# Optimization experiments

Hardware: AMD Instinct MI355X
Metric: run time of the kernel (lower is better)

## Reference

```python
import jax, jax.numpy as jnp
import numpy as np

B, S, H, A = 32, 4096, 512, 256

def setup_inputs() -> dict:
    key = jax.random.key(0)
    ks = jax.random.split(key, 8)
    sH = 1.0 / np.sqrt(H)
    sA = 1.0 / np.sqrt(A)
    return {
        "encoder_outputs": jax.random.normal(ks[0], (B, S, H), dtype=jnp.float32),
        "decoder_hidden": jax.random.normal(ks[1], (B, H), dtype=jnp.float32),
        "W_enc": jax.random.uniform(ks[2], (H, A), jnp.float32, -sH, sH),
        "b_enc": jax.random.uniform(ks[3], (A,), jnp.float32, -sH, sH),
        "W_dec": jax.random.uniform(ks[4], (H, A), jnp.float32, -sH, sH),
        "b_dec": jax.random.uniform(ks[5], (A,), jnp.float32, -sH, sH),
        "W_e": jax.random.uniform(ks[6], (A,), jnp.float32, -sA, sA),
        "b_e": jax.random.uniform(ks[7], (), jnp.float32, -sA, sA),
    }

def reference(encoder_outputs, decoder_hidden, W_enc, b_enc, W_dec, b_dec, W_e, b_e):
    # [B,S,A] encoder projection
    enc_p = jnp.einsum('bsh,ha->bsa', encoder_outputs, W_enc) + b_enc
    # [B,1,A] decoder projection broadcast over S
    dec_p = (decoder_hidden @ W_dec + b_dec)[:, None, :]
    scores = jnp.einsum('bsa,a->bs', jnp.tanh(enc_p + dec_p), W_e) + b_e  # [B,S]
    attn = jax.nn.softmax(scores, axis=1)                                 # [B,S]
    context = jnp.einsum('bs,bsh->bh', attn, encoder_outputs)             # [B,H]
    return context, attn
```

## Files before the change

kernel.cpp:

```cpp
#include <hip/hip_runtime.h>
#include <hip/hip_bf16.h>
#include <stdint.h>


typedef __attribute__((ext_vector_type(4))) float f32x4;
typedef __attribute__((ext_vector_type(8))) short short8;

#define B_  32
#define S_  4096
#define H_  512
#define A_  256
#define CHUNKS_ 64

#define WS_WT     0
#define WS_BIAS   262144
#define WS_SCORES 294912
#define WS_M      819200
#define WS_L      827392
#define WS_PART   835584

#define STRIDE_ 520

static __device__ __forceinline__ short f2bf(float f) {
  union { float f; uint32_t u; } v; v.f = f;
  uint32_t r = (v.u + 0x7FFFu + ((v.u >> 16) & 1u)) >> 16;
  return (short)(uint16_t)r;
}
static __device__ __forceinline__ float bf2f(uint32_t lo16) {
  union { uint32_t u; float f; } v; v.u = lo16 << 16; return v.f;
}

static __device__ __forceinline__ void lds_barrier() {
  asm volatile("s_waitcnt lgkmcnt(0)" ::: "memory");
  __builtin_amdgcn_s_barrier();
  asm volatile("" ::: "memory");
}

__global__ __launch_bounds__(256) void prep_kernel(
    const float* __restrict__ dh, const float* __restrict__ W_enc,
    const float* __restrict__ b_enc, const float* __restrict__ W_dec,
    const float* __restrict__ b_dec, unsigned short* __restrict__ WT,
    float* __restrict__ bias) {
  __shared__ float dh_s[512];
  __shared__ unsigned short tile[64 * 66];
  const int tid = threadIdx.x;
  if (blockIdx.x < 32) {
    const int b = blockIdx.x;
    dh_s[tid]       = dh[(size_t)b * H_ + tid];
    dh_s[tid + 256] = dh[(size_t)b * H_ + tid + 256];
    __syncthreads();
    float s[4] = {0.f, 0.f, 0.f, 0.f};
    for (int k = 0; k < H_; k += 32) {
      #pragma unroll
      for (int j = 0; j < 32; ++j)
        s[j & 3] = fmaf(dh_s[k + j], W_dec[(size_t)(k + j) * A_ + tid], s[j & 3]);
    }
    bias[b * A_ + tid] = s[0] + s[1] + s[2] + s[3] + b_enc[tid] + b_dec[tid];
  } else {
    const int t = blockIdx.x - 32;
    const int kt = t >> 2, nt2 = t & 3;
    #pragma unroll
    for (int i = 0; i < 16; ++i) {
      int idx = tid + i * 256;
      int kk = idx >> 6, nn = idx & 63;
      tile[kk * 66 + nn] =
          (unsigned short)f2bf(W_enc[(size_t)(kt * 64 + kk) * A_ + nt2 * 64 + nn]);
    }
    __syncthreads();
    #pragma unroll
    for (int i = 0; i < 16; ++i) {
      int idx = tid + i * 256;
      int nn = idx >> 6, kk = idx & 63;
      WT[(size_t)(nt2 * 64 + nn) * H_ + kt * 64 + kk] = tile[kk * 66 + nn];
    }
  }
}

__global__ __launch_bounds__(256, 2) void fused_kernel(
    const float* __restrict__ enc, const unsigned short* __restrict__ WT,
    const float* __restrict__ bias, const float* __restrict__ We,
    float* __restrict__ scores, float* __restrict__ wsm,
    float* __restrict__ wsl, float* __restrict__ part) {
  __shared__ __align__(16) unsigned short stash[64 * STRIDE_];
  __shared__ float s_ps[4][64];
  __shared__ float s_e[64];

  const int tid = threadIdx.x, w = tid >> 6, lane = tid & 63;
  const int lm = lane & 15, lq = lane >> 4;
  const int b = blockIdx.x >> 6;
  const int chunk = blockIdx.x & 63;
  const int srow0 = blockIdx.x * 64;

  f32x4 acc[4][4];
  #pragma unroll
  for (int mt = 0; mt < 4; ++mt)
    #pragma unroll
    for (int nt = 0; nt < 4; ++nt)
      acc[mt][nt] = (f32x4){0.f, 0.f, 0.f, 0.f};

  const int arow = tid >> 2, akoff = (tid & 3) * 8;
  const float* aptr = enc + (size_t)(srow0 + arow) * H_ + akoff;
  unsigned short* swp = &stash[arow * STRIDE_ + akoff];

  const unsigned short* bptr = WT + (size_t)((w * 4) * 16 + lm) * H_ + lq * 8;

  short8 Bring[3][4];
  float4 Aring[3][2];

  float4 a0a = *(const float4*)aptr;
  float4 a0b = *(const float4*)(aptr + 4);
  Aring[1][0] = *(const float4*)(aptr + 1 * 32);
  Aring[1][1] = *(const float4*)(aptr + 1 * 32 + 4);
  Aring[2][0] = *(const float4*)(aptr + 2 * 32);
  Aring[2][1] = *(const float4*)(aptr + 2 * 32 + 4);
  #pragma unroll
  for (int j = 0; j < 4; ++j) {
    Bring[0][j] = *(const short8*)(bptr + (size_t)j * 16 * H_);
    Bring[1][j] = *(const short8*)(bptr + (size_t)j * 16 * H_ + 32);
  }
  {
    short8 sv;
    sv[0] = f2bf(a0a.x); sv[1] = f2bf(a0a.y); sv[2] = f2bf(a0a.z); sv[3] = f2bf(a0a.w);
    sv[4] = f2bf(a0b.x); sv[5] = f2bf(a0b.y); sv[6] = f2bf(a0b.z); sv[7] = f2bf(a0b.w);
    *(short8*)swp = sv;
  }
  lds_barrier();

  #pragma unroll
  for (int k = 0; k < 16; ++k) {
    if (k + 3 < 16) {
      Aring[(k + 3) % 3][0] = *(const float4*)(aptr + (k + 3) * 32);
      Aring[(k + 3) % 3][1] = *(const float4*)(aptr + (k + 3) * 32 + 4);
    }
    if (k + 2 < 16) {
      #pragma unroll
      for (int j = 0; j < 4; ++j)
        Bring[(k + 2) % 3][j] = *(const short8*)(bptr + (size_t)j * 16 * H_ + (k + 2) * 32);
    }
    #pragma unroll
    for (int mt = 0; mt < 4; ++mt) {
      short8 af = *(const short8*)&stash[(mt * 16 + lm) * STRIDE_ + k * 32 + lq * 8];
      #pragma unroll
      for (int j = 0; j < 4; ++j)
        acc[mt][j] = __builtin_amdgcn_mfma_f32_16x16x32_bf16(af, Bring[k % 3][j], acc[mt][j], 0, 0, 0);
    }
    if (k < 15) {
      float4 ca = Aring[(k + 1) % 3][0];
      float4 cb = Aring[(k + 1) % 3][1];
      short8 sv;
      sv[0] = f2bf(ca.x); sv[1] = f2bf(ca.y); sv[2] = f2bf(ca.z); sv[3] = f2bf(ca.w);
      sv[4] = f2bf(cb.x); sv[5] = f2bf(cb.y); sv[6] = f2bf(cb.z); sv[7] = f2bf(cb.w);
      *(short8*)(swp + (k + 1) * 32) = sv;
      lds_barrier();
    }
  }

  float psum[4][4] = {{0,0,0,0},{0,0,0,0},{0,0,0,0},{0,0,0,0}};
  #pragma unroll
  for (int j = 0; j < 4; ++j) {
    const int col = (w * 4 + j) * 16 + lm;
    const float dp = bias[b * A_ + col];
    const float wv = We[col];
    #pragma unroll
    for (int mt = 0; mt < 4; ++mt)
      #pragma unroll
      for (int r = 0; r < 4; ++r) {
        float x = acc[mt][j][r] + dp;
        float e = __expf(2.0f * x);
        float t = 1.0f - 2.0f * __builtin_amdgcn_rcpf(e + 1.0f);
        psum[mt][r] = fmaf(t, wv, psum[mt][r]);
      }
  }
  #pragma unroll
  for (int o = 1; o < 16; o <<= 1)
    #pragma unroll
    for (int mt = 0; mt < 4; ++mt)
      #pragma unroll
      for (int r = 0; r < 4; ++r)
        psum[mt][r] += __shfl_xor(psum[mt][r], o, 64);
  if (lm == 0) {
    #pragma unroll
    for (int mt = 0; mt < 4; ++mt)
      #pragma unroll
      for (int r = 0; r < 4; ++r)
        s_ps[w][mt * 16 + lq * 4 + r] = psum[mt][r];
  }
  lds_barrier();

  if (tid < 64) {
    const float sc = s_ps[0][tid] + s_ps[1][tid] + s_ps[2][tid] + s_ps[3][tid];
    float m = sc;
    #pragma unroll
    for (int o = 1; o < 64; o <<= 1) m = fmaxf(m, __shfl_xor(m, o, 64));
    const float e = __expf(sc - m);
    float l = e;
    #pragma unroll
    for (int o = 1; o < 64; o <<= 1) l += __shfl_xor(l, o, 64);
    s_e[tid] = e;
    scores[srow0 + tid] = e;
    if (tid == 0) {
      wsm[b * CHUNKS_ + chunk] = m;
      wsl[b * CHUNKS_ + chunk] = l;
    }
  }
  lds_barrier();

  float cx0 = 0.f, cx1 = 0.f;
  #pragma unroll 8
  for (int row = 0; row < 64; ++row) {
    uint32_t pv = *(const uint32_t*)&stash[row * STRIDE_ + (tid << 1)];
    float wr = s_e[row];
    cx0 = fmaf(wr, bf2f(pv & 0xffffu), cx0);
    cx1 = fmaf(wr, bf2f(pv >> 16), cx1);
  }
  float2 o2; o2.x = cx0; o2.y = cx1;
  *(float2*)&part[(size_t)(b * CHUNKS_ + chunk) * H_ + (tid << 1)] = o2;
}

__global__ __launch_bounds__(256) void finalize_kernel(
    const float* __restrict__ scores_e, const float* __restrict__ wsm,
    const float* __restrict__ wsl, const float* __restrict__ part,
    float* __restrict__ ctx, float* __restrict__ attn) {
  __shared__ float wgt[CHUNKS_];
  __shared__ float s_inv;
  __shared__ float csum[4][64];
  const int b = blockIdx.x >> 3, j = blockIdx.x & 7;
  const int tid = threadIdx.x;
  if (tid < 64) {
    float mc = wsm[b * CHUNKS_ + tid];
    float lc = wsl[b * CHUNKS_ + tid];
    float M = mc;
    #pragma unroll
    for (int o = 1; o < 64; o <<= 1) M = fmaxf(M, __shfl_xor(M, o, 64));
    float wv = __expf(mc - M);
    float Lp = wv * lc;
    #pragma unroll
    for (int o = 1; o < 64; o <<= 1) Lp += __shfl_xor(Lp, o, 64);
    wgt[tid] = wv;
    if (tid == 0) s_inv = 1.0f / Lp;
  }
  __syncthreads();
  const float invL = s_inv;

  {
    const int h = j * 64 + (tid & 63), g = tid >> 6;
    float s = 0.f;
    #pragma unroll 4
    for (int c = g * 16; c < g * 16 + 16; ++c)
      s = fmaf(wgt[c], part[(size_t)(b * CHUNKS_ + c) * H_ + h], s);
    csum[g][tid & 63] = s;
  }
  __syncthreads();
  if (tid < 64) {
    float s = csum[0][tid] + csum[1][tid] + csum[2][tid] + csum[3][tid];
    ctx[(size_t)b * H_ + j * 64 + tid] = s * invL;
  }

  #pragma unroll
  for (int i = 0; i < 2; ++i) {
    const int s_ = j * 512 + tid + i * 256;
    attn[(size_t)b * S_ + s_] = scores_e[(size_t)b * S_ + s_] * wgt[s_ >> 6] * invL;
  }
}

extern "C" void kernel_launch(void* const* d_in, const int* in_sizes, int n_in,
                              void* d_out, int out_size, void* d_ws, size_t ws_size,
                              hipStream_t stream) {
  const float* enc   = (const float*)d_in[0];
  const float* dh    = (const float*)d_in[1];
  const float* W_enc = (const float*)d_in[2];
  const float* b_enc = (const float*)d_in[3];
  const float* W_dec = (const float*)d_in[4];
  const float* b_dec = (const float*)d_in[5];
  const float* W_e   = (const float*)d_in[6];

  char* ws = (char*)d_ws;
  unsigned short* WT = (unsigned short*)(ws + WS_WT);
  float* bias   = (float*)(ws + WS_BIAS);
  float* scores = (float*)(ws + WS_SCORES);
  float* wsm    = (float*)(ws + WS_M);
  float* wsl    = (float*)(ws + WS_L);
  float* part   = (float*)(ws + WS_PART);

  float* ctx  = (float*)d_out;
  float* attn = (float*)d_out + B_ * H_;

  prep_kernel<<<dim3(64), dim3(256), 0, stream>>>(dh, W_enc, b_enc, W_dec, b_dec, WT, bias);
  fused_kernel<<<dim3(2048), dim3(256), 0, stream>>>(enc, WT, bias, W_e, scores, wsm, wsl, part);
  finalize_kernel<<<dim3(256), dim3(256), 0, stream>>>(scores, wsm, wsl, part, ctx, attn);
}
```

Measured before the change: 414.2 us.

## Make fused kernel persistent over four tiles with cross-tile prefetch and packed bf16 convert

Result: slower. 430.9 us (+4.0%).

```diff
diff --git a/kernel.cpp b/kernel.cpp
--- a/kernel.cpp
+++ b/kernel.cpp
@@ -5,6 +5,7 @@
 
 typedef __attribute__((ext_vector_type(4))) float f32x4;
 typedef __attribute__((ext_vector_type(8))) short short8;
+typedef __attribute__((ext_vector_type(4))) uint32_t u32x4;
 
 #define B_  32
 #define S_  4096
@@ -28,6 +29,11 @@
 }
 static __device__ __forceinline__ float bf2f(uint32_t lo16) {
   union { uint32_t u; float f; } v; v.u = lo16 << 16; return v.f;
+}
+static __device__ __forceinline__ uint32_t cvt_pk_bf16(float a, float b) {
+  uint32_t r;
+  asm("v_cvt_pk_bf16_f32 %0, %1, %2" : "=v"(r) : "v"(a), "v"(b));
+  return r;
 }
 
 static __device__ __forceinline__ void lds_barrier() {
@@ -87,28 +93,20 @@
 
   const int tid = threadIdx.x, w = tid >> 6, lane = tid & 63;
   const int lm = lane & 15, lq = lane >> 4;
-  const int b = blockIdx.x >> 6;
-  const int chunk = blockIdx.x & 63;
-  const int srow0 = blockIdx.x * 64;
-
-  f32x4 acc[4][4];
-  #pragma unroll
-  for (int mt = 0; mt < 4; ++mt)
-    #pragma unroll
-    for (int nt = 0; nt < 4; ++nt)
-      acc[mt][nt] = (f32x4){0.f, 0.f, 0.f, 0.f};
 
   const int arow = tid >> 2, akoff = (tid & 3) * 8;
-  const float* aptr = enc + (size_t)(srow0 + arow) * H_ + akoff;
   unsigned short* swp = &stash[arow * STRIDE_ + akoff];
 
   const unsigned short* bptr = WT + (size_t)((w * 4) * 16 + lm) * H_ + lq * 8;
 
   short8 Bring[3][4];
   float4 Aring[3][2];
-
-  float4 a0a = *(const float4*)aptr;
-  float4 a0b = *(const float4*)(aptr + 4);
+  float4 a0a, a0b;
+
+  int g = blockIdx.x;
+  const float* aptr = enc + (size_t)(g * 64 + arow) * H_ + akoff;
+  a0a = *(const float4*)aptr;
+  a0b = *(const float4*)(aptr + 4);
   Aring[1][0] = *(const float4*)(aptr + 1 * 32);
   Aring[1][1] = *(const float4*)(aptr + 1 * 32 + 4);
   Aring[2][0] = *(const float4*)(aptr + 2 * 32);
@@ -118,103 +116,136 @@
     Bring[0][j] = *(const short8*)(bptr + (size_t)j * 16 * H_);
     Bring[1][j] = *(const short8*)(bptr + (size_t)j * 16 * H_ + 32);
   }
-  {
-    short8 sv;
-    sv[0] = f2bf(a0a.x); sv[1] = f2bf(a0a.y); sv[2] = f2bf(a0a.z); sv[3] = f2bf(a0a.w);
-    sv[4] = f2bf(a0b.x); sv[5] = f2bf(a0b.y); sv[6] = f2bf(a0b.z); sv[7] = f2bf(a0b.w);
-    *(short8*)swp = sv;
-  }
-  lds_barrier();
-
-  #pragma unroll
-  for (int k = 0; k < 16; ++k) {
-    if (k + 3 < 16) {
-      Aring[(k + 3) % 3][0] = *(const float4*)(aptr + (k + 3) * 32);
-      Aring[(k + 3) % 3][1] = *(const float4*)(aptr + (k + 3) * 32 + 4);
-    }
-    if (k + 2 < 16) {
-      #pragma unroll
-      for (int j = 0; j < 4; ++j)
-        Bring[(k + 2) % 3][j] = *(const short8*)(bptr + (size_t)j * 16 * H_ + (k + 2) * 32);
-    }
-    #pragma unroll
-    for (int mt = 0; mt < 4; ++mt) {
-      short8 af = *(const short8*)&stash[(mt * 16 + lm) * STRIDE_ + k * 32 + lq * 8];
-      #pragma unroll
-      for (int j = 0; j < 4; ++j)
-        acc[mt][j] = __builtin_amdgcn_mfma_f32_16x16x32_bf16(af, Bring[k % 3][j], acc[mt][j], 0, 0, 0);
-    }
-    if (k < 15) {
-      float4 ca = Aring[(k + 1) % 3][0];
-      float4 cb = Aring[(k + 1) % 3][1];
-      short8 sv;
-      sv[0] = f2bf(ca.x); sv[1] = f2bf(ca.y); sv[2] = f2bf(ca.z); sv[3] = f2bf(ca.w);
-      sv[4] = f2bf(cb.x); sv[5] = f2bf(cb.y); sv[6] = f2bf(cb.z); sv[7] = f2bf(cb.w);
-      *(short8*)(swp + (k + 1) * 32) = sv;
-      lds_barrier();
-    }
-  }
-
-  float psum[4][4] = {{0,0,0,0},{0,0,0,0},{0,0,0,0},{0,0,0,0}};
-  #pragma unroll
-  for (int j = 0; j < 4; ++j) {
-    const int col = (w * 4 + j) * 16 + lm;
-    const float dp = bias[b * A_ + col];
-    const float wv = We[col];
+
+  for (int it = 0; ; ++it) {
+    const int b = g >> 6, chunk = g & 63;
+    const int srow0 = g * 64;
+
+    {
+      u32x4 sv;
+      sv.x = cvt_pk_bf16(a0a.x, a0a.y); sv.y = cvt_pk_bf16(a0a.z, a0a.w);
+      sv.z = cvt_pk_bf16(a0b.x, a0b.y); sv.w = cvt_pk_bf16(a0b.z, a0b.w);
+      *(u32x4*)swp = sv;
+    }
+    lds_barrier();
+
+    f32x4 acc[4][4];
     #pragma unroll
     for (int mt = 0; mt < 4; ++mt)
       #pragma unroll
-      for (int r = 0; r < 4; ++r) {
-        float x = acc[mt][j][r] + dp;
-        float e = __expf(2.0f * x);
-        float t = 1.0f - 2.0f * __builtin_amdgcn_rcpf(e + 1.0f);
-        psum[mt][r] = fmaf(t, wv, psum[mt][r]);
-      }
-  }
-  #pragma unroll
-  for (int o = 1; o < 16; o <<= 1)
-    #pragma unroll
-    for (int mt = 0; mt < 4; ++mt)
-      #pragma unroll
-      for (int r = 0; r < 4; ++r)
-        psum[mt][r] += __shfl_xor(psum[mt][r], o, 64);
-  if (lm == 0) {
-    #pragma unroll
-    for (int mt = 0; mt < 4; ++mt)
-      #pragma unroll
-      for (int r = 0; r < 4; ++r)
-        s_ps[w][mt * 16 + lq * 4 + r] = psum[mt][r];
-  }
-  lds_barrier();
-
-  if (tid < 64) {
-    const float sc = s_ps[0][tid] + s_ps[1][tid] + s_ps[2][tid] + s_ps[3][tid];
-    float m = sc;
-    #pragma unroll
-    for (int o = 1; o < 64; o <<= 1) m = fmaxf(m, __shfl_xor(m, o, 64));
-    const float e = __expf(sc - m);
-    float l = e;
-    #pragma unroll
-    for (int o = 1; o < 64; o <<= 1) l += __shfl_xor(l, o, 64);
-    s_e[tid] = e;
-    scores[srow0 + tid] = e;
-    if (tid == 0) {
-      wsm[b * CHUNKS_ + chunk] = m;
-      wsl[b * CHUNKS_ + chunk] = l;
-    }
-  }
-  lds_barrier();
-
-  float cx0 = 0.f, cx1 = 0.f;
-  #pragma unroll 8
-  for (int row = 0; row < 64; ++row) {
-    uint32_t pv = *(const uint32_t*)&stash[row * STRIDE_ + (tid << 1)];
-    float wr = s_e[row];
-    cx0 = fmaf(wr, bf2f(pv & 0xffffu), cx0);
-    cx1 = fmaf(wr, bf2f(pv >> 16), cx1);
-  }
-  float2 o2; o2.x = cx0; o2.y = cx1;
-  *(float2*)&part[(size_t)(b * CHUNKS_ + chunk) * H_ + (tid << 1)] = o2;
+      for (int nt = 0; nt < 4; ++nt)
+        acc[mt][nt] = (f32x4){0.f, 0.f, 0.f, 0.f};
+
+    #pragma unroll
+    for (int k = 0; k < 16; ++k) {
+      if (k + 3 < 16) {
+        Aring[(k + 3) % 3][0] = *(const float4*)(aptr + (k + 3) * 32);
+        Aring[(k + 3) % 3][1] = *(const float4*)(aptr + (k + 3) * 32 + 4);
+      }
+      if (k + 2 < 16) {
+        #pragma unroll
+        for (int j = 0; j < 4; ++j)
+          Bring[(k + 2) % 3][j] = *(const short8*)(bptr + (size_t)j * 16 * H_ + (k + 2) * 32);
+      }
+      #pragma unroll
+      for (int mt = 0; mt < 4; ++mt) {
+        short8 af = *(const short8*)&stash[(mt * 16 + lm) * STRIDE_ + k * 32 + lq * 8];
+        #pragma unroll
+        for (int j = 0; j < 4; ++j)
+          acc[mt][j] = __builtin_amdgcn_mfma_f32_16x16x32_bf16(af, Bring[k % 3][j], acc[mt][j], 0, 0, 0);
+      }
+      if (k < 15) {
+        float4 ca = Aring[(k + 1) % 3][0];
+        float4 cb = Aring[(k + 1) % 3][1];
+        u32x4 sv;
+        sv.x = cvt_pk_bf16(ca.x, ca.y); sv.y = cvt_pk_bf16(ca.z, ca.w);
+        sv.z = cvt_pk_bf16(cb.x, cb.y); sv.w = cvt_pk_bf16(cb.z, cb.w);
+        *(u32x4*)(swp + (k + 1) * 32) = sv;
+        lds_barrier();
+      }
+    }
+
+    if (it < 3) {
+      const int gn = g + 512;
+      aptr = enc + (size_t)(gn * 64 + arow) * H_ + akoff;
+      a0a = *(const float4*)aptr;
+      a0b = *(const float4*)(aptr + 4);
+      Aring[1][0] = *(const float4*)(aptr + 1 * 32);
+      Aring[1][1] = *(const float4*)(aptr + 1 * 32 + 4);
+      Aring[2][0] = *(const float4*)(aptr + 2 * 32);
+      Aring[2][1] = *(const float4*)(aptr + 2 * 32 + 4);
+      #pragma unroll
+      for (int j = 0; j < 4; ++j) {
+        Bring[0][j] = *(const short8*)(bptr + (size_t)j * 16 * H_);
+        Bring[1][j] = *(const short8*)(bptr + (size_t)j * 16 * H_ + 32);
+      }
+    }
+
+    float psum[4][4] = {{0,0,0,0},{0,0,0,0},{0,0,0,0},{0,0,0,0}};
+    #pragma unroll
+    for (int j = 0; j < 4; ++j) {
+      const int col = (w * 4 + j) * 16 + lm;
+      const float dp = bias[b * A_ + col];
+      const float wv = We[col];
+      #pragma unroll
+      for (int mt = 0; mt < 4; ++mt)
+        #pragma unroll
+        for (int r = 0; r < 4; ++r) {
+          float x = acc[mt][j][r] + dp;
+          float e = __expf(2.0f * x);
+          float t = 1.0f - 2.0f * __builtin_amdgcn_rcpf(e + 1.0f);
+          psum[mt][r] = fmaf(t, wv, psum[mt][r]);
+        }
+    }
+    #pragma unroll
+    for (int o = 1; o < 16; o <<= 1)
+      #pragma unroll
+      for (int mt = 0; mt < 4; ++mt)
+        #pragma unroll
+        for (int r = 0; r < 4; ++r)
+          psum[mt][r] += __shfl_xor(psum[mt][r], o, 64);
+    if (lm == 0) {
+      #pragma unroll
+      for (int mt = 0; mt < 4; ++mt)
+        #pragma unroll
+        for (int r = 0; r < 4; ++r)
+          s_ps[w][mt * 16 + lq * 4 + r] = psum[mt][r];
+    }
+    lds_barrier();
+
+    if (tid < 64) {
+      const float sc = s_ps[0][tid] + s_ps[1][tid] + s_ps[2][tid] + s_ps[3][tid];
+      float m = sc;
+      #pragma unroll
+      for (int o = 1; o < 64; o <<= 1) m = fmaxf(m, __shfl_xor(m, o, 64));
+      const float e = __expf(sc - m);
+      float l = e;
+      #pragma unroll
+      for (int o = 1; o < 64; o <<= 1) l += __shfl_xor(l, o, 64);
+      s_e[tid] = e;
+      scores[srow0 + tid] = e;
+      if (tid == 0) {
+        wsm[b * CHUNKS_ + chunk] = m;
+        wsl[b * CHUNKS_ + chunk] = l;
+      }
+    }
+    lds_barrier();
+
+    float cx0 = 0.f, cx1 = 0.f;
+    #pragma unroll 8
+    for (int row = 0; row < 64; ++row) {
+      uint32_t pv = *(const uint32_t*)&stash[row * STRIDE_ + (tid << 1)];
+      float wr = s_e[row];
+      cx0 = fmaf(wr, bf2f(pv & 0xffffu), cx0);
+      cx1 = fmaf(wr, bf2f(pv >> 16), cx1);
+    }
+    float2 o2; o2.x = cx0; o2.y = cx1;
+    *(float2*)&part[(size_t)(b * CHUNKS_ + chunk) * H_ + (tid << 1)] = o2;
+
+    if (it == 3) break;
+    g += 512;
+    lds_barrier();
+  }
 }
 
 __global__ __launch_bounds__(256) void finalize_kernel(
@@ -243,12 +274,12 @@
   const float invL = s_inv;
 
   {
-    const int h = j * 64 + (tid & 63), g = tid >> 6;
+    const int h = j * 64 + (tid & 63), gq = tid >> 6;
     float s = 0.f;
     #pragma unroll 4
-    for (int c = g * 16; c < g * 16 + 16; ++c)
+    for (int c = gq * 16; c < gq * 16 + 16; ++c)
       s = fmaf(wgt[c], part[(size_t)(b * CHUNKS_ + c) * H_ + h], s);
-    csum[g][tid & 63] = s;
+    csum[gq][tid & 63] = s;
   }
   __syncthreads();
   if (tid < 64) {
@@ -286,6 +317,6 @@
   float* attn = (float*)d_out + B_ * H_;
 
   prep_kernel<<<dim3(64), dim3(256), 0, stream>>>(dh, W_enc, b_enc, W_dec, b_dec, WT, bias);
-  fused_kernel<<<dim3(2048), dim3(256), 0, stream>>>(enc, WT, bias, W_e, scores, wsm, wsl, part);
+  fused_kernel<<<dim3(512), dim3(256), 0, stream>>>(enc, WT, bias, W_e, scores, wsm, wsl, part);
   finalize_kernel<<<dim3(256), dim3(256), 0, stream>>>(scores, wsm, wsl, part, ctx, attn);
 }
```
